# Kernel optimization log

Measured on AMD Instinct MI355X. Metric: run time of the kernel, lower is better.

Reference implementation:

```python
import jax, jax.numpy as jnp
import numpy as np

N_NODES = 50000
N_EDGES = 1200000
IN_DIM = 140
EDGE_DIM = 3
EMB = 64
L = 4
BN_EPS = 1e-5


def _bn(x, gamma, beta):
    # BatchNorm1d in training mode: batch statistics over axis 0 (biased var)
    mu = jnp.mean(x, axis=0)
    var = jnp.var(x, axis=0)
    return (x - mu) * jax.lax.rsqrt(var + BN_EPS) * gamma + beta


def setup_inputs() -> dict:
    key = jax.random.key(0)
    ks = jax.random.split(key, 24)
    s = lambda *sh: 0.05
    inp = {
        "x": jax.random.normal(ks[0], (N_NODES, IN_DIM), jnp.float32),
        "edge_index": jax.random.randint(ks[1], (2, N_EDGES), 0, N_NODES, jnp.int32),
        "edge_attr": jax.random.normal(ks[2], (N_EDGES, EDGE_DIM), jnp.float32),
        "lin_in_w": jax.random.normal(ks[3], (IN_DIM, EMB), jnp.float32) * 0.05,
        "lin_in_b": jnp.zeros((EMB,), jnp.float32),
        "ee_w1": jax.random.normal(ks[4], (L, EDGE_DIM, EMB), jnp.float32) * 0.1,
        "ee_b1": jnp.zeros((L, EMB), jnp.float32),
        "ee_g1": jnp.ones((L, EMB), jnp.float32),
        "ee_be1": jnp.zeros((L, EMB), jnp.float32),
        "ee_w2": jax.random.normal(ks[5], (L, EMB, EMB), jnp.float32) * 0.05,
        "ee_b2": jnp.zeros((L, EMB), jnp.float32),
        "mlp_w1": jax.random.normal(ks[6], (L, EMB, EMB), jnp.float32) * 0.05,
        "mlp_b1": jnp.zeros((L, EMB), jnp.float32),
        "mlp_g1": jnp.ones((L, EMB), jnp.float32),
        "mlp_be1": jnp.zeros((L, EMB), jnp.float32),
        "mlp_w2": jax.random.normal(ks[7], (L, EMB, EMB), jnp.float32) * 0.05,
        "mlp_b2": jnp.zeros((L, EMB), jnp.float32),
        "mlp_g2": jnp.ones((L, EMB), jnp.float32),
        "mlp_be2": jnp.zeros((L, EMB), jnp.float32),
        "lin_pred_w": jax.random.normal(ks[8], (EMB, 1), jnp.float32) * 0.05,
        "lin_pred_b": jnp.zeros((1,), jnp.float32),
    }
    return inp


def reference(x, edge_index, edge_attr, lin_in_w, lin_in_b,
              ee_w1, ee_b1, ee_g1, ee_be1, ee_w2, ee_b2,
              mlp_w1, mlp_b1, mlp_g1, mlp_be1, mlp_w2, mlp_b2, mlp_g2, mlp_be2,
              lin_pred_w, lin_pred_b):
    src, dst = edge_index[0], edge_index[1]
    n = x.shape[0]
    h = x @ lin_in_w + lin_in_b  # [N, EMB]
    for l in range(L):
        # edge encoder: Linear -> BN -> ReLU -> Linear
        e = edge_attr @ ee_w1[l] + ee_b1[l]
        e = jax.nn.relu(_bn(e, ee_g1[l], ee_be1[l]))
        e = e @ ee_w2[l] + ee_b2[l]  # [E, EMB]
        agg_e = jax.ops.segment_sum(e, dst, num_segments=n)
        hh = h + agg_e
        # GINConv (eps=0): mlp(hh + sum_{j->i} hh_j)
        msg = jax.ops.segment_sum(hh[src], dst, num_segments=n)
        z = hh + msg
        z = jax.nn.relu(_bn(z @ mlp_w1[l] + mlp_b1[l], mlp_g1[l], mlp_be1[l]))
        z = jax.nn.relu(_bn(z @ mlp_w2[l] + mlp_b2[l], mlp_g2[l], mlp_be2[l]))
        h = h + z  # residual in GINModel.forward
    out = h @ lin_pred_w + lin_pred_b
    return out[:, 0]
```

## Files before the change

### kernel.cpp

```cpp
#include <hip/hip_runtime.h>

#define EMB 64
#define INDIM 140
#define NL 4
#define EPS 1e-5f

__device__ __forceinline__ float bnrelu(float v, float sum, float sq, float g, float be, float invN){
  float mu  = sum*invN;
  float var = fmaf(-mu, mu, sq*invN);
  float sc  = g * rsqrtf(var + EPS);
  return fmaxf(fmaf(v - mu, sc, be), 0.f);
}

__global__ __launch_bounds__(256) void k_pass1(const int* __restrict__ dst,
    const float* __restrict__ ea, int E, int* __restrict__ deg, float* __restrict__ est)
{
  __shared__ float ls[9];
  if (threadIdx.x < 9) ls[threadIdx.x] = 0.f;
  __syncthreads();
  int tid = blockIdx.x*blockDim.x + threadIdx.x;
  int stride = gridDim.x*blockDim.x;
  float a0=0,a1=0,a2=0,p00=0,p11=0,p22=0,p01=0,p02=0,p12=0;
  for (int e=tid;e<E;e+=stride){
    atomicAdd(&deg[dst[e]],1);
    float d0=ea[3*e+0], d1=ea[3*e+1], d2=ea[3*e+2];
    a0+=d0;a1+=d1;a2+=d2;
    p00=fmaf(d0,d0,p00); p11=fmaf(d1,d1,p11); p22=fmaf(d2,d2,p22);
    p01=fmaf(d0,d1,p01); p02=fmaf(d0,d2,p02); p12=fmaf(d1,d2,p12);
  }
  #pragma unroll
  for (int off=32; off>0; off>>=1){
    a0+=__shfl_down(a0,off); a1+=__shfl_down(a1,off); a2+=__shfl_down(a2,off);
    p00+=__shfl_down(p00,off); p11+=__shfl_down(p11,off); p22+=__shfl_down(p22,off);
    p01+=__shfl_down(p01,off); p02+=__shfl_down(p02,off); p12+=__shfl_down(p12,off);
  }
  if ((threadIdx.x & 63)==0){
    atomicAdd(&ls[0],a0); atomicAdd(&ls[1],a1); atomicAdd(&ls[2],a2);
    atomicAdd(&ls[3],p00); atomicAdd(&ls[4],p11); atomicAdd(&ls[5],p22);
    atomicAdd(&ls[6],p01); atomicAdd(&ls[7],p02); atomicAdd(&ls[8],p12);
  }
  __syncthreads();
  if (threadIdx.x < 9) atomicAdd(&est[threadIdx.x*16], ls[threadIdx.x]);
}

__global__ __launch_bounds__(256) void k_scanA(const int* __restrict__ deg,
    int* __restrict__ bsum, int n)
{
  int b = blockIdx.x, t = threadIdx.x;
  int i0 = b*1024 + t*4;
  int s = 0;
  if (i0+3 < n){ int4 v = *(const int4*)(deg+i0); s = v.x+v.y+v.z+v.w; }
  else { for (int j=0;j<4;j++){ int i=i0+j; if (i<n) s += deg[i]; } }
  #pragma unroll
  for (int off=32;off>0;off>>=1) s += __shfl_down(s, off);
  __shared__ int ws[4];
  if ((t&63)==0) ws[t>>6] = s;
  __syncthreads();
  if (t==0) bsum[b] = ws[0]+ws[1]+ws[2]+ws[3];
}

__global__ __launch_bounds__(64) void k_scanB(const int* __restrict__ bsum,
    int* __restrict__ boff, int* __restrict__ rs, int nb, int n)
{
  int t = threadIdx.x;
  int carry = 0;
  for (int base=0; base<nb; base+=64){
    int idx = base + t;
    int v = (idx<nb)? bsum[idx] : 0;
    int x = v;
    #pragma unroll
    for (int off=1;off<64;off<<=1){ int u = __shfl_up(x, off); if (t>=off) x += u; }
    if (idx<nb) boff[idx] = carry + x - v;
    int tot = __shfl(x, 63);
    carry += tot;
  }
  if (t==0) rs[n] = carry;
}

__global__ __launch_bounds__(256) void k_scanC(int* __restrict__ deg,
    const int* __restrict__ boff, int* __restrict__ rs, int n)
{
  int b = blockIdx.x, t = threadIdx.x;
  int i0 = b*1024 + t*4;
  int a=0,c=0,d=0,e=0;
  if (i0+3 < n){ int4 v = *(const int4*)(deg+i0); a=v.x;c=v.y;d=v.z;e=v.w; }
  else { if(i0<n)a=deg[i0]; if(i0+1<n)c=deg[i0+1]; if(i0+2<n)d=deg[i0+2]; if(i0+3<n)e=deg[i0+3]; }
  int s4 = a+c+d+e;
  int x = s4;
  int lane = t & 63;
  #pragma unroll
  for (int off=1;off<64;off<<=1){ int u = __shfl_up(x, off); if (lane>=off) x += u; }
  int wexcl = x - s4;
  __shared__ int ws[4];
  if (lane==63) ws[t>>6] = x;
  __syncthreads();
  int base = boff[b];
  int wid = t>>6;
  for (int j=0;j<wid;j++) base += ws[j];
  int p = base + wexcl;
  int r0=p, r1=p+a, r2=p+a+c, r3=p+a+c+d;
  if (i0+3 < n){
    *(int4*)(rs+i0)  = make_int4(r0,r1,r2,r3);
    *(int4*)(deg+i0) = make_int4(r0,r1,r2,r3);
  } else {
    if(i0<n){rs[i0]=r0;deg[i0]=r0;} if(i0+1<n){rs[i0+1]=r1;deg[i0+1]=r1;}
    if(i0+2<n){rs[i0+2]=r2;deg[i0+2]=r2;} if(i0+3<n){rs[i0+3]=r3;deg[i0+3]=r3;}
  }
}

__global__ __launch_bounds__(256) void k_scatter(const int* __restrict__ src,
    const int* __restrict__ dst, const float* __restrict__ ea, int E,
    int* __restrict__ cur, float4* __restrict__ rec)
{
  int tid = blockIdx.x*blockDim.x + threadIdx.x;
  int stride = gridDim.x*blockDim.x;
  for (int e=tid;e<E;e+=stride){
    int d = dst[e];
    int p = atomicAdd(&cur[d], 1);
    rec[p] = make_float4(ea[3*e+0], ea[3*e+1], ea[3*e+2], (float)src[e]);
  }
}

__global__ __launch_bounds__(256) void k_prec(const float* __restrict__ est,
  const float* __restrict__ w1, const float* __restrict__ b1,
  const float* __restrict__ g1, const float* __restrict__ be1,
  float* __restrict__ ac, float invE)
{
  int t = threadIdx.x; int l = t>>6, c = t&63;
  float m0 = est[0]*invE, m1 = est[16]*invE, m2 = est[32]*invE;
  float c00 = est[48]*invE - m0*m0, c11 = est[64]*invE - m1*m1, c22 = est[80]*invE - m2*m2;
  float c01 = est[96]*invE - m0*m1, c02 = est[112]*invE - m0*m2, c12 = est[128]*invE - m1*m2;
  float w0 = w1[(l*3+0)*64+c], w1_ = w1[(l*3+1)*64+c], w2_ = w1[(l*3+2)*64+c];
  float b = b1[l*64+c], g = g1[l*64+c], be = be1[l*64+c];
  float mu = m0*w0 + m1*w1_ + m2*w2_ + b;
  float var = w0*w0*c00 + w1_*w1_*c11 + w2_*w2_*c22
            + 2.f*(w0*w1_*c01 + w0*w2_*c02 + w1_*w2_*c12);
  float sc = g * rsqrtf(var + EPS);
  float* o = ac + l*256 + c*4;
  o[0] = w0*sc; o[1] = w1_*sc; o[2] = w2_*sc; o[3] = (b - mu)*sc + be;
}

__global__ __launch_bounds__(256) void k_h0(const float* __restrict__ x,
  const float* __restrict__ w, const float* __restrict__ b, float* __restrict__ h, int n)
{
  __shared__ float4 s_x[4][280];
  int wv = (blockIdx.x*256 + threadIdx.x) >> 6;
  int wslot = (threadIdx.x >> 6) & 3;
  int lane = threadIdx.x & 63;
  int i0 = wv*8;
  int m = n - i0; if (m > 8) m = 8; if (m < 0) m = 0;
  int limit = m*35;
  const float4* xp4 = (const float4*)(x + (size_t)i0*INDIM);
  #pragma unroll
  for (int j=0;j<5;j++){
    int idx = j*64 + lane;
    if (idx < limit) s_x[wslot][idx] = xp4[idx];
  }
  __syncthreads();
  float acc[8];
  float bl = b[lane];
  #pragma unroll
  for (int t=0;t<8;t++) acc[t] = bl;
  const float* wcol = w + lane;
  #pragma unroll 1
  for (int kq=0; kq<35; kq++){
    float w0 = wcol[(4*kq+0)*EMB];
    float w1 = wcol[(4*kq+1)*EMB];
    float w2 = wcol[(4*kq+2)*EMB];
    float w3 = wcol[(4*kq+3)*EMB];
    #pragma unroll
    for (int t=0;t<8;t++){
      float4 xv = s_x[wslot][t*35 + kq];
      acc[t] = fmaf(xv.x, w0, acc[t]);
      acc[t] = fmaf(xv.y, w1, acc[t]);
      acc[t] = fmaf(xv.z, w2, acc[t]);
      acc[t] = fmaf(xv.w, w3, acc[t]);
    }
  }
  #pragma unroll
  for (int t=0;t<8;t++)
    if (t < m) h[(size_t)(i0+t)*EMB + lane] = acc[t];
}

__global__ __launch_bounds__(256) void k_l1(
  float* __restrict__ h, float* __restrict__ hh, const float* __restrict__ yprev,
  const int* __restrict__ rs, const float4* __restrict__ rec,
  const float* __restrict__ ac, const float* __restrict__ w2, const float* __restrict__ b2,
  const float* __restrict__ st2, const float* __restrict__ g2, const float* __restrict__ be2,
  int n, int update, float invN)
{
  __shared__ float4 ldsr[4][4][16];
  int wv = (blockIdx.x*256 + threadIdx.x) >> 6;
  int wslot = (threadIdx.x >> 6) & 3;
  int lane = threadIdx.x & 63;
  int i0 = wv*4;
  float4 a = ((const float4*)ac)[lane];
  float b2l = b2[lane];
  float accv[4];
  #pragma unroll
  for (int t=0;t<4;t++){
    int i = i0 + t;
    bool act = (i < n);
    int ii = act ? i : 0;
    int e0 = rs[ii], e1 = rs[ii+1];
    float racc = 0.f;
    int e = e0;
    for (; e+8<=e1; e+=8){
      float4 d0 = rec[e],   d1 = rec[e+1], d2 = rec[e+2], d3 = rec[e+3];
      float4 d4 = rec[e+4], d5 = rec[e+5], d6 = rec[e+6], d7 = rec[e+7];
      racc += fmaxf(fmaf(d0.x,a.x,fmaf(d0.y,a.y,fmaf(d0.z,a.z,a.w))),0.f);
      racc += fmaxf(fmaf(d1.x,a.x,fmaf(d1.y,a.y,fmaf(d1.z,a.z,a.w))),0.f);
      racc += fmaxf(fmaf(d2.x,a.x,fmaf(d2.y,a.y,fmaf(d2.z,a.z,a.w))),0.f);
      racc += fmaxf(fmaf(d3.x,a.x,fmaf(d3.y,a.y,fmaf(d3.z,a.z,a.w))),0.f);
      racc += fmaxf(fmaf(d4.x,a.x,fmaf(d4.y,a.y,fmaf(d4.z,a.z,a.w))),0.f);
      racc += fmaxf(fmaf(d5.x,a.x,fmaf(d5.y,a.y,fmaf(d5.z,a.z,a.w))),0.f);
      racc += fmaxf(fmaf(d6.x,a.x,fmaf(d6.y,a.y,fmaf(d6.z,a.z,a.w))),0.f);
      racc += fmaxf(fmaf(d7.x,a.x,fmaf(d7.y,a.y,fmaf(d7.z,a.z,a.w))),0.f);
    }
    for (; e<e1; e++){
      float4 d0 = rec[e];
      racc += fmaxf(fmaf(d0.x,a.x,fmaf(d0.y,a.y,fmaf(d0.z,a.z,a.w))),0.f);
    }
    ((float*)&ldsr[wslot][t])[lane] = racc;
    float hv = h[(size_t)ii*EMB + lane];
    if (update){
      float yv = yprev[(size_t)ii*EMB + lane];
      hv += bnrelu(yv, st2[lane*16], st2[(64+lane)*16], g2[lane], be2[lane], invN);
      if (act) h[(size_t)i*EMB + lane] = hv;
    }
    float degf = (float)(e1 - e0);
    accv[t] = fmaf(degf, b2l, hv);
  }
  __syncthreads();
  const float* wcol = w2 + lane;
  #pragma unroll 1
  for (int kq=0; kq<16; kq++){
    float w0 = wcol[(4*kq+0)*EMB];
    float w1v = wcol[(4*kq+1)*EMB];
    float w2v = wcol[(4*kq+2)*EMB];
    float w3 = wcol[(4*kq+3)*EMB];
    #pragma unroll
    for (int t=0;t<4;t++){
      float4 rv = ldsr[wslot][t][kq];
      accv[t] = fmaf(rv.x, w0, accv[t]);
      accv[t] = fmaf(rv.y, w1v, accv[t]);
      accv[t] = fmaf(rv.z, w2v, accv[t]);
      accv[t] = fmaf(rv.w, w3, accv[t]);
    }
  }
  #pragma unroll
  for (int t=0;t<4;t++)
    if (i0+t < n) hh[(size_t)(i0+t)*EMB + lane] = accv[t];
}

__global__ __launch_bounds__(256) void k_l2(
  const float* __restrict__ hh, const int* __restrict__ rs, const float* __restrict__ recw,
  const float* __restrict__ w1, const float* __restrict__ b1,
  float* __restrict__ y, float* __restrict__ pst, int n)
{
  __shared__ float4 ldsz[4][4][16];
  __shared__ float ls[128];
  int wv = (blockIdx.x*256 + threadIdx.x) >> 6;
  int wslot = (threadIdx.x >> 6) & 3;
  int lane = threadIdx.x & 63;
  int i0 = wv*4;
  if (threadIdx.x < 128) ls[threadIdx.x] = 0.f;
  #pragma unroll
  for (int t=0;t<4;t++){
    int i = i0 + t;
    bool act = (i < n);
    int ii = act ? i : 0;
    int e0 = rs[ii], e1 = rs[ii+1];
    float zc = hh[(size_t)ii*EMB + lane];
    int e = e0;
    for (; e+8<=e1; e+=8){
      int s0 = (int)recw[4*(e+0)+3];
      int s1 = (int)recw[4*(e+1)+3];
      int s2 = (int)recw[4*(e+2)+3];
      int s3 = (int)recw[4*(e+3)+3];
      int s4 = (int)recw[4*(e+4)+3];
      int s5 = (int)recw[4*(e+5)+3];
      int s6 = (int)recw[4*(e+6)+3];
      int s7 = (int)recw[4*(e+7)+3];
      float g0 = hh[(size_t)s0*EMB + lane];
      float g1 = hh[(size_t)s1*EMB + lane];
      float g2 = hh[(size_t)s2*EMB + lane];
      float g3 = hh[(size_t)s3*EMB + lane];
      float g4 = hh[(size_t)s4*EMB + lane];
      float g5 = hh[(size_t)s5*EMB + lane];
      float g6 = hh[(size_t)s6*EMB + lane];
      float g7 = hh[(size_t)s7*EMB + lane];
      zc += ((g0+g1)+(g2+g3)) + ((g4+g5)+(g6+g7));
    }
    for (; e<e1; e++){
      int s0 = (int)recw[4*e+3];
      zc += hh[(size_t)s0*EMB + lane];
    }
    ((float*)&ldsz[wslot][t])[lane] = zc;
  }
  __syncthreads();
  float b1l = b1[lane];
  float accv[4];
  #pragma unroll
  for (int t=0;t<4;t++) accv[t] = b1l;
  const float* wcol = w1 + lane;
  #pragma unroll 1
  for (int kq=0; kq<16; kq++){
    float w0 = wcol[(4*kq+0)*EMB];
    float w1v = wcol[(4*kq+1)*EMB];
    float w2v = wcol[(4*kq+2)*EMB];
    float w3 = wcol[(4*kq+3)*EMB];
    #pragma unroll
    for (int t=0;t<4;t++){
      float4 zv = ldsz[wslot][t][kq];
      accv[t] = fmaf(zv.x, w0, accv[t]);
      accv[t] = fmaf(zv.y, w1v, accv[t]);
      accv[t] = fmaf(zv.z, w2v, accv[t]);
      accv[t] = fmaf(zv.w, w3, accv[t]);
    }
  }
  float ssum = 0.f, ssq = 0.f;
  #pragma unroll
  for (int t=0;t<4;t++){
    if (i0+t < n){
      y[(size_t)(i0+t)*EMB + lane] = accv[t];
      ssum += accv[t];
      ssq = fmaf(accv[t], accv[t], ssq);
    }
  }
  atomicAdd(&ls[lane], ssum); atomicAdd(&ls[64+lane], ssq);
  __syncthreads();
  if (threadIdx.x < 128) pst[(size_t)blockIdx.x*128 + threadIdx.x] = ls[threadIdx.x];
}

__global__ __launch_bounds__(256) void k_l3(float* __restrict__ y,
  const float* __restrict__ st1, const float* __restrict__ g1, const float* __restrict__ be1,
  const float* __restrict__ w2, const float* __restrict__ b2,
  float* __restrict__ pst, int n, float invN)
{
  __shared__ float4 ldst[4][4][16];
  __shared__ float ls[128];
  int wv = (blockIdx.x*256 + threadIdx.x) >> 6;
  int wslot = (threadIdx.x >> 6) & 3;
  int lane = threadIdx.x & 63;
  int i0 = wv*4;
  if (threadIdx.x < 128) ls[threadIdx.x] = 0.f;
  float s1 = st1[lane*16], sq1 = st1[(64+lane)*16];
  float g1l = g1[lane], be1l = be1[lane];
  #pragma unroll
  for (int t=0;t<4;t++){
    int i = i0 + t;
    int ii = (i < n) ? i : 0;
    float yv = y[(size_t)ii*EMB + lane];
    ((float*)&ldst[wslot][t])[lane] = bnrelu(yv, s1, sq1, g1l, be1l, invN);
  }
  __syncthreads();
  float b2l = b2[lane];
  float accv[4];
  #pragma unroll
  for (int t=0;t<4;t++) accv[t] = b2l;
  const float* wcol = w2 + lane;
  #pragma unroll 1
  for (int kq=0; kq<16; kq++){
    float w0 = wcol[(4*kq+0)*EMB];
    float w1v = wcol[(4*kq+1)*EMB];
    float w2v = wcol[(4*kq+2)*EMB];
    float w3 = wcol[(4*kq+3)*EMB];
    #pragma unroll
    for (int t=0;t<4;t++){
      float4 tv = ldst[wslot][t][kq];
      accv[t] = fmaf(tv.x, w0, accv[t]);
      accv[t] = fmaf(tv.y, w1v, accv[t]);
      accv[t] = fmaf(tv.z, w2v, accv[t]);
      accv[t] = fmaf(tv.w, w3, accv[t]);
    }
  }
  float ssum = 0.f, ssq = 0.f;
  #pragma unroll
  for (int t=0;t<4;t++){
    if (i0+t < n){
      y[(size_t)(i0+t)*EMB + lane] = accv[t];
      ssum += accv[t];
      ssq = fmaf(accv[t], accv[t], ssq);
    }
  }
  atomicAdd(&ls[lane], ssum); atomicAdd(&ls[64+lane], ssq);
  __syncthreads();
  if (threadIdx.x < 128) pst[(size_t)blockIdx.x*128 + threadIdx.x] = ls[threadIdx.x];
}

__global__ __launch_bounds__(256) void k_red(const float* __restrict__ pst,
    float* __restrict__ st, int nb)
{
  int ch = blockIdx.x;
  float s = 0.f;
  for (int i=threadIdx.x; i<nb; i+=256) s += pst[(size_t)i*128 + ch];
  #pragma unroll
  for (int off=32; off>0; off>>=1) s += __shfl_down(s, off);
  __shared__ float ws[4];
  if ((threadIdx.x&63)==0) ws[threadIdx.x>>6] = s;
  __syncthreads();
  if (threadIdx.x==0) st[ch*16] = ws[0]+ws[1]+ws[2]+ws[3];
}

__global__ __launch_bounds__(64) void k_out(
  const float* __restrict__ h, const float* __restrict__ y,
  const float* __restrict__ st2, const float* __restrict__ g2, const float* __restrict__ be2,
  const float* __restrict__ wp, const float* __restrict__ bp,
  float* __restrict__ out, int n, float invN)
{
  int i = blockIdx.x*64 + threadIdx.x; if (i>=n) return;
  const float* hr = h + (size_t)i*EMB;
  const float* yr = y + (size_t)i*EMB;
  float acc = 0.f;
  #pragma unroll
  for (int q=0;q<16;q++){
    int c0=q*4;
    float4 hv = *(const float4*)(hr+c0);
    float4 yv = *(const float4*)(yr+c0);
    float f0 = hv.x + bnrelu(yv.x, st2[(c0+0)*16], st2[(64+c0+0)*16], g2[c0+0], be2[c0+0], invN);
    float f1 = hv.y + bnrelu(yv.y, st2[(c0+1)*16], st2[(64+c0+1)*16], g2[c0+1], be2[c0+1], invN);
    float f2 = hv.z + bnrelu(yv.z, st2[(c0+2)*16], st2[(64+c0+2)*16], g2[c0+2], be2[c0+2], invN);
    float f3 = hv.w + bnrelu(yv.w, st2[(c0+3)*16], st2[(64+c0+3)*16], g2[c0+3], be2[c0+3], invN);
    acc = fmaf(f0, wp[c0+0], acc);
    acc = fmaf(f1, wp[c0+1], acc);
    acc = fmaf(f2, wp[c0+2], acc);
    acc = fmaf(f3, wp[c0+3], acc);
  }
  out[i] = acc + bp[0];
}

extern "C" void kernel_launch(void* const* d_in, const int* in_sizes, int n_in,
                              void* d_out, int out_size, void* d_ws, size_t ws_size,
                              hipStream_t stream)
{
  const float* x        = (const float*)d_in[0];
  const int*   ei       = (const int*)d_in[1];
  const float* ea       = (const float*)d_in[2];
  const float* lin_in_w = (const float*)d_in[3];
  const float* lin_in_b = (const float*)d_in[4];
  const float* ee_w1    = (const float*)d_in[5];
  const float* ee_b1    = (const float*)d_in[6];
  const float* ee_g1    = (const float*)d_in[7];
  const float* ee_be1   = (const float*)d_in[8];
  const float* ee_w2    = (const float*)d_in[9];
  const float* ee_b2    = (const float*)d_in[10];
  const float* mlp_w1   = (const float*)d_in[11];
  const float* mlp_b1   = (const float*)d_in[12];
  const float* mlp_g1   = (const float*)d_in[13];
  const float* mlp_be1  = (const float*)d_in[14];
  const float* mlp_w2   = (const float*)d_in[15];
  const float* mlp_b2   = (const float*)d_in[16];
  const float* mlp_g2   = (const float*)d_in[17];
  const float* mlp_be2  = (const float*)d_in[18];
  const float* pred_w   = (const float*)d_in[19];
  const float* pred_b   = (const float*)d_in[20];

  int n = in_sizes[0] / INDIM;
  int E = in_sizes[1] / 2;
  const int* srcp = ei;
  const int* dstp = ei + E;

  char* w = (char*)d_ws;
  auto al = [](size_t o){ return (o + 255) & ~(size_t)255; };
  size_t o = 0;
  int*   deg = (int*)(w + o);  o += (size_t)n*4;  o = al(o);
  float* est = (float*)(w + o); o += 144*4;  o = al(o);
  size_t zero_bytes = o;
  o = al(o); float* nst = (float*)(w + o); o += (size_t)NL*2*2048*4;
  o = al(o); int* rs   = (int*)(w + o);   o += (size_t)(n+1)*4;
  o = al(o); int* bsum = (int*)(w + o);   o += 256*4;
  o = al(o); int* boff = (int*)(w + o);   o += 256*4;
  o = al(o); float4* rec = (float4*)(w + o); o += (size_t)E*16;
  o = al(o); float* acb = (float*)(w + o); o += (size_t)NL*256*4;
  o = al(o); float* h   = (float*)(w + o); o += (size_t)n*EMB*4;
  o = al(o); float* hhb = (float*)(w + o); o += (size_t)n*EMB*4;
  o = al(o); float* yb  = (float*)(w + o); o += (size_t)n*EMB*4;
  o = al(o); float* pst = (float*)(w + o); o += (size_t)4096*128*4;

  (void)hipMemsetAsync(d_ws, 0, zero_bytes, stream);

  int nbChunk = (n + 1023)/1024;
  k_pass1<<<512, 256, 0, stream>>>(dstp, ea, E, deg, est);
  k_scanA<<<nbChunk, 256, 0, stream>>>(deg, bsum, n);
  k_scanB<<<1, 64, 0, stream>>>(bsum, boff, rs, nbChunk, n);
  k_scanC<<<nbChunk, 256, 0, stream>>>(deg, boff, rs, n);
  k_scatter<<<1024, 256, 0, stream>>>(srcp, dstp, ea, E, deg , rec);
  k_prec<<<1, 256, 0, stream>>>(est, ee_w1, ee_b1, ee_g1, ee_be1, acb, 1.f/(float)E);

  int nb_h0 = ((n + 7)/8 + 3)/4;
  int nb_l  = (n + 15)/16;
  float invN = 1.f/(float)n;
  k_h0<<<nb_h0, 256, 0, stream>>>(x, lin_in_w, lin_in_b, h, n);

  for (int l=0; l<NL; l++){
    float* st1 = nst + (size_t)l*4096;
    float* st2 = st1 + 2048;
    const float* st2prev = (l>0) ? (nst + (size_t)(l-1)*4096 + 2048) : nst;
    const float* g2p  = (l>0) ? (mlp_g2  + (size_t)(l-1)*64) : mlp_g2;
    const float* be2p = (l>0) ? (mlp_be2 + (size_t)(l-1)*64) : mlp_be2;
    k_l1<<<nb_l, 256, 0, stream>>>(h, hhb, yb, rs, rec,
        acb + (size_t)l*256, ee_w2 + (size_t)l*4096, ee_b2 + (size_t)l*64,
        st2prev, g2p, be2p, n, (l>0)?1:0, invN);
    k_l2<<<nb_l, 256, 0, stream>>>(hhb, rs, (const float*)rec,
        mlp_w1 + (size_t)l*4096, mlp_b1 + (size_t)l*64, yb, pst, n);
    k_red<<<128, 256, 0, stream>>>(pst, st1, nb_l);
    k_l3<<<nb_l, 256, 0, stream>>>(yb, st1,
        mlp_g1 + (size_t)l*64, mlp_be1 + (size_t)l*64,
        mlp_w2 + (size_t)l*4096, mlp_b2 + (size_t)l*64, pst, n, invN);
    k_red<<<128, 256, 0, stream>>>(pst, st2, nb_l);
  }
  k_out<<<(n+63)/64, 64, 0, stream>>>(h, yb,
      nst + (size_t)(NL-1)*4096 + 2048, mlp_g2 + (size_t)(NL-1)*64, mlp_be2 + (size_t)(NL-1)*64,
      pred_w, pred_b, (float*)d_out, n, invN);
}
```

Baseline: 961.4 us.

## Store hh in bf16, precompute CSR ranks, tweak unrolls and output block size

Several changes at once. The intermediate hh buffer is now stored as bf16, which halves the bytes read by the gather in k_l2, the dominant random-access traffic. Each edge's rank within its destination is recorded during degree counting, so the scatter needs no second atomic pass. The BN parameter loads in k_l1 are hoisted out of the per-node loop and the h update moves ahead of the edge loop. GEMM loops get unroll 2 and k_out uses 256-thread blocks. The bf16 storage lowers precision of the aggregated features, and the rank array adds E*4 bytes of traffic.

```diff
diff --git a/kernel.cpp b/kernel.cpp
--- a/kernel.cpp
+++ b/kernel.cpp
@@ -1,9 +1,19 @@
 #include <hip/hip_runtime.h>
+#include <hip/hip_bf16.h>
 
 #define EMB 64
 #define INDIM 140
 #define NL 4
 #define EPS 1e-5f
+
+__device__ __forceinline__ unsigned short f2bf(float f){
+  __hip_bfloat16 b = __float2bfloat16(f);
+  return *reinterpret_cast<unsigned short*>(&b);
+}
+__device__ __forceinline__ float bf2f(unsigned short u){
+  __hip_bfloat16 b = *reinterpret_cast<__hip_bfloat16*>(&u);
+  return __bfloat162float(b);
+}
 
 __device__ __forceinline__ float bnrelu(float v, float sum, float sq, float g, float be, float invN){
   float mu  = sum*invN;
@@ -13,7 +23,8 @@
 }
 
 __global__ __launch_bounds__(256) void k_pass1(const int* __restrict__ dst,
-    const float* __restrict__ ea, int E, int* __restrict__ deg, float* __restrict__ est)
+    const float* __restrict__ ea, int E, int* __restrict__ deg,
+    int* __restrict__ rank, float* __restrict__ est)
 {
   __shared__ float ls[9];
   if (threadIdx.x < 9) ls[threadIdx.x] = 0.f;
@@ -22,7 +33,7 @@
   int stride = gridDim.x*blockDim.x;
   float a0=0,a1=0,a2=0,p00=0,p11=0,p22=0,p01=0,p02=0,p12=0;
   for (int e=tid;e<E;e+=stride){
-    atomicAdd(&deg[dst[e]],1);
+    rank[e] = atomicAdd(&deg[dst[e]],1);
     float d0=ea[3*e+0], d1=ea[3*e+1], d2=ea[3*e+2];
     a0+=d0;a1+=d1;a2+=d2;
     p00=fmaf(d0,d0,p00); p11=fmaf(d1,d1,p11); p22=fmaf(d2,d2,p22);
@@ -101,22 +112,20 @@
   int r0=p, r1=p+a, r2=p+a+c, r3=p+a+c+d;
   if (i0+3 < n){
     *(int4*)(rs+i0)  = make_int4(r0,r1,r2,r3);
-    *(int4*)(deg+i0) = make_int4(r0,r1,r2,r3);
   } else {
-    if(i0<n){rs[i0]=r0;deg[i0]=r0;} if(i0+1<n){rs[i0+1]=r1;deg[i0+1]=r1;}
-    if(i0+2<n){rs[i0+2]=r2;deg[i0+2]=r2;} if(i0+3<n){rs[i0+3]=r3;deg[i0+3]=r3;}
+    if(i0<n)rs[i0]=r0; if(i0+1<n)rs[i0+1]=r1;
+    if(i0+2<n)rs[i0+2]=r2; if(i0+3<n)rs[i0+3]=r3;
   }
 }
 
 __global__ __launch_bounds__(256) void k_scatter(const int* __restrict__ src,
     const int* __restrict__ dst, const float* __restrict__ ea, int E,
-    int* __restrict__ cur, float4* __restrict__ rec)
+    const int* __restrict__ rs, const int* __restrict__ rank, float4* __restrict__ rec)
 {
   int tid = blockIdx.x*blockDim.x + threadIdx.x;
   int stride = gridDim.x*blockDim.x;
   for (int e=tid;e<E;e+=stride){
-    int d = dst[e];
-    int p = atomicAdd(&cur[d], 1);
+    int p = rs[dst[e]] + rank[e];
     rec[p] = make_float4(ea[3*e+0], ea[3*e+1], ea[3*e+2], (float)src[e]);
   }
 }
@@ -162,7 +171,7 @@
   #pragma unroll
   for (int t=0;t<8;t++) acc[t] = bl;
   const float* wcol = w + lane;
-  #pragma unroll 1
+  #pragma unroll 2
   for (int kq=0; kq<35; kq++){
     float w0 = wcol[(4*kq+0)*EMB];
     float w1 = wcol[(4*kq+1)*EMB];
@@ -183,7 +192,7 @@
 }
 
 __global__ __launch_bounds__(256) void k_l1(
-  float* __restrict__ h, float* __restrict__ hh, const float* __restrict__ yprev,
+  float* __restrict__ h, unsigned short* __restrict__ hh16, const float* __restrict__ yprev,
   const int* __restrict__ rs, const float4* __restrict__ rec,
   const float* __restrict__ ac, const float* __restrict__ w2, const float* __restrict__ b2,
   const float* __restrict__ st2, const float* __restrict__ g2, const float* __restrict__ be2,
@@ -196,6 +205,8 @@
   int i0 = wv*4;
   float4 a = ((const float4*)ac)[lane];
   float b2l = b2[lane];
+  float s2s = 0.f, s2q = 0.f, g2l = 0.f, be2l = 0.f;
+  if (update){ s2s = st2[lane*16]; s2q = st2[(64+lane)*16]; g2l = g2[lane]; be2l = be2[lane]; }
   float accv[4];
   #pragma unroll
   for (int t=0;t<4;t++){
@@ -203,6 +214,12 @@
     bool act = (i < n);
     int ii = act ? i : 0;
     int e0 = rs[ii], e1 = rs[ii+1];
+    float hv = h[(size_t)ii*EMB + lane];
+    if (update){
+      float yv = yprev[(size_t)ii*EMB + lane];
+      hv += bnrelu(yv, s2s, s2q, g2l, be2l, invN);
+      if (act) h[(size_t)i*EMB + lane] = hv;
+    }
     float racc = 0.f;
     int e = e0;
     for (; e+8<=e1; e+=8){
@@ -222,18 +239,12 @@
       racc += fmaxf(fmaf(d0.x,a.x,fmaf(d0.y,a.y,fmaf(d0.z,a.z,a.w))),0.f);
     }
     ((float*)&ldsr[wslot][t])[lane] = racc;
-    float hv = h[(size_t)ii*EMB + lane];
-    if (update){
-      float yv = yprev[(size_t)ii*EMB + lane];
-      hv += bnrelu(yv, st2[lane*16], st2[(64+lane)*16], g2[lane], be2[lane], invN);
-      if (act) h[(size_t)i*EMB + lane] = hv;
-    }
     float degf = (float)(e1 - e0);
     accv[t] = fmaf(degf, b2l, hv);
   }
   __syncthreads();
   const float* wcol = w2 + lane;
-  #pragma unroll 1
+  #pragma unroll 2
   for (int kq=0; kq<16; kq++){
     float w0 = wcol[(4*kq+0)*EMB];
     float w1v = wcol[(4*kq+1)*EMB];
@@ -250,11 +261,11 @@
   }
   #pragma unroll
   for (int t=0;t<4;t++)
-    if (i0+t < n) hh[(size_t)(i0+t)*EMB + lane] = accv[t];
+    if (i0+t < n) hh16[(size_t)(i0+t)*EMB + lane] = f2bf(accv[t]);
 }
 
 __global__ __launch_bounds__(256) void k_l2(
-  const float* __restrict__ hh, const int* __restrict__ rs, const float* __restrict__ recw,
+  const unsigned short* __restrict__ hh16, const int* __restrict__ rs, const float* __restrict__ recw,
   const float* __restrict__ w1, const float* __restrict__ b1,
   float* __restrict__ y, float* __restrict__ pst, int n)
 {
@@ -271,7 +282,7 @@
     bool act = (i < n);
     int ii = act ? i : 0;
     int e0 = rs[ii], e1 = rs[ii+1];
-    float zc = hh[(size_t)ii*EMB + lane];
+    float zc = bf2f(hh16[(size_t)ii*EMB + lane]);
     int e = e0;
     for (; e+8<=e1; e+=8){
       int s0 = (int)recw[4*(e+0)+3];
@@ -282,19 +293,19 @@
       int s5 = (int)recw[4*(e+5)+3];
       int s6 = (int)recw[4*(e+6)+3];
       int s7 = (int)recw[4*(e+7)+3];
-      float g0 = hh[(size_t)s0*EMB + lane];
-      float g1 = hh[(size_t)s1*EMB + lane];
-      float g2 = hh[(size_t)s2*EMB + lane];
-      float g3 = hh[(size_t)s3*EMB + lane];
-      float g4 = hh[(size_t)s4*EMB + lane];
-      float g5 = hh[(size_t)s5*EMB + lane];
-      float g6 = hh[(size_t)s6*EMB + lane];
-      float g7 = hh[(size_t)s7*EMB + lane];
+      float g0 = bf2f(hh16[(size_t)s0*EMB + lane]);
+      float g1 = bf2f(hh16[(size_t)s1*EMB + lane]);
+      float g2 = bf2f(hh16[(size_t)s2*EMB + lane]);
+      float g3 = bf2f(hh16[(size_t)s3*EMB + lane]);
+      float g4 = bf2f(hh16[(size_t)s4*EMB + lane]);
+      float g5 = bf2f(hh16[(size_t)s5*EMB + lane]);
+      float g6 = bf2f(hh16[(size_t)s6*EMB + lane]);
+      float g7 = bf2f(hh16[(size_t)s7*EMB + lane]);
       zc += ((g0+g1)+(g2+g3)) + ((g4+g5)+(g6+g7));
     }
     for (; e<e1; e++){
       int s0 = (int)recw[4*e+3];
-      zc += hh[(size_t)s0*EMB + lane];
+      zc += bf2f(hh16[(size_t)s0*EMB + lane]);
     }
     ((float*)&ldsz[wslot][t])[lane] = zc;
   }
@@ -304,7 +315,7 @@
   #pragma unroll
   for (int t=0;t<4;t++) accv[t] = b1l;
   const float* wcol = w1 + lane;
-  #pragma unroll 1
+  #pragma unroll 2
   for (int kq=0; kq<16; kq++){
     float w0 = wcol[(4*kq+0)*EMB];
     float w1v = wcol[(4*kq+1)*EMB];
@@ -360,7 +371,7 @@
   #pragma unroll
   for (int t=0;t<4;t++) accv[t] = b2l;
   const float* wcol = w2 + lane;
-  #pragma unroll 1
+  #pragma unroll 2
   for (int kq=0; kq<16; kq++){
     float w0 = wcol[(4*kq+0)*EMB];
     float w1v = wcol[(4*kq+1)*EMB];
@@ -403,13 +414,13 @@
   if (threadIdx.x==0) st[ch*16] = ws[0]+ws[1]+ws[2]+ws[3];
 }
 
-__global__ __launch_bounds__(64) void k_out(
+__global__ __launch_bounds__(256) void k_out(
   const float* __restrict__ h, const float* __restrict__ y,
   const float* __restrict__ st2, const float* __restrict__ g2, const float* __restrict__ be2,
   const float* __restrict__ wp, const float* __restrict__ bp,
   float* __restrict__ out, int n, float invN)
 {
-  int i = blockIdx.x*64 + threadIdx.x; if (i>=n) return;
+  int i = blockIdx.x*256 + threadIdx.x; if (i>=n) return;
   const float* hr = h + (size_t)i*EMB;
   const float* yr = y + (size_t)i*EMB;
   float acc = 0.f;
@@ -471,21 +482,22 @@
   o = al(o); int* rs   = (int*)(w + o);   o += (size_t)(n+1)*4;
   o = al(o); int* bsum = (int*)(w + o);   o += 256*4;
   o = al(o); int* boff = (int*)(w + o);   o += 256*4;
+  o = al(o); int* rank = (int*)(w + o);   o += (size_t)E*4;
   o = al(o); float4* rec = (float4*)(w + o); o += (size_t)E*16;
   o = al(o); float* acb = (float*)(w + o); o += (size_t)NL*256*4;
   o = al(o); float* h   = (float*)(w + o); o += (size_t)n*EMB*4;
-  o = al(o); float* hhb = (float*)(w + o); o += (size_t)n*EMB*4;
+  o = al(o); unsigned short* hh16 = (unsigned short*)(w + o); o += (size_t)n*EMB*2;
   o = al(o); float* yb  = (float*)(w + o); o += (size_t)n*EMB*4;
   o = al(o); float* pst = (float*)(w + o); o += (size_t)4096*128*4;
 
   (void)hipMemsetAsync(d_ws, 0, zero_bytes, stream);
 
   int nbChunk = (n + 1023)/1024;
-  k_pass1<<<512, 256, 0, stream>>>(dstp, ea, E, deg, est);
+  k_pass1<<<512, 256, 0, stream>>>(dstp, ea, E, deg, rank, est);
   k_scanA<<<nbChunk, 256, 0, stream>>>(deg, bsum, n);
   k_scanB<<<1, 64, 0, stream>>>(bsum, boff, rs, nbChunk, n);
   k_scanC<<<nbChunk, 256, 0, stream>>>(deg, boff, rs, n);
-  k_scatter<<<1024, 256, 0, stream>>>(srcp, dstp, ea, E, deg , rec);
+  k_scatter<<<1024, 256, 0, stream>>>(srcp, dstp, ea, E, rs, rank, rec);
   k_prec<<<1, 256, 0, stream>>>(est, ee_w1, ee_b1, ee_g1, ee_be1, acb, 1.f/(float)E);
 
   int nb_h0 = ((n + 7)/8 + 3)/4;
@@ -499,10 +511,10 @@
     const float* st2prev = (l>0) ? (nst + (size_t)(l-1)*4096 + 2048) : nst;
     const float* g2p  = (l>0) ? (mlp_g2  + (size_t)(l-1)*64) : mlp_g2;
     const float* be2p = (l>0) ? (mlp_be2 + (size_t)(l-1)*64) : mlp_be2;
-    k_l1<<<nb_l, 256, 0, stream>>>(h, hhb, yb, rs, rec,
+    k_l1<<<nb_l, 256, 0, stream>>>(h, hh16, yb, rs, rec,
         acb + (size_t)l*256, ee_w2 + (size_t)l*4096, ee_b2 + (size_t)l*64,
         st2prev, g2p, be2p, n, (l>0)?1:0, invN);
-    k_l2<<<nb_l, 256, 0, stream>>>(hhb, rs, (const float*)rec,
+    k_l2<<<nb_l, 256, 0, stream>>>(hh16, rs, (const float*)rec,
         mlp_w1 + (size_t)l*4096, mlp_b1 + (size_t)l*64, yb, pst, n);
     k_red<<<128, 256, 0, stream>>>(pst, st1, nb_l);
     k_l3<<<nb_l, 256, 0, stream>>>(yb, st1,
@@ -510,7 +522,7 @@
         mlp_w2 + (size_t)l*4096, mlp_b2 + (size_t)l*64, pst, n, invN);
     k_red<<<128, 256, 0, stream>>>(pst, st2, nb_l);
   }
-  k_out<<<(n+63)/64, 64, 0, stream>>>(h, yb,
+  k_out<<<(n+255)/256, 256, 0, stream>>>(h, yb,
       nst + (size_t)(NL-1)*4096 + 2048, mlp_g2 + (size_t)(NL-1)*64, mlp_be2 + (size_t)(NL-1)*64,
       pred_w, pred_b, (float*)d_out, n, invN);
 }
```

New measurement: 816.6 us. 15.1% less time.
